# Performance work log

Hardware: AMD Instinct MI355X
Metric: run time of the kernel (lower is better)

The kernel has to match this reference:

```python
import jax, jax.numpy as jnp
import numpy as np

N_NODES = 50000
N_EDGES = 1600000
IN_FEAT = 128
HIDDEN = 128
NUM_CLASSES = 10
NUM_GRAPHS = 128


def setup_inputs() -> dict:
    key = jax.random.key(0)
    ks = jax.random.split(key, 10)
    x = jax.random.normal(ks[0], (N_NODES, IN_FEAT), dtype=jnp.float32)
    edge_index = jax.random.randint(ks[1], (2, N_EDGES), 0, N_NODES, dtype=jnp.int64)
    batch = jnp.sort(jax.random.randint(ks[2], (N_NODES,), 0, NUM_GRAPHS, dtype=jnp.int64))
    edge_mask = jax.random.uniform(ks[3], (N_EDGES,), dtype=jnp.float32)
    # Glorot-ish init for weights, zeros for biases (PyG default: glorot W, zero bias)
    def glorot(k, fan_in, fan_out):
        s = jnp.sqrt(6.0 / (fan_in + fan_out))
        return jax.random.uniform(k, (fan_in, fan_out), minval=-s, maxval=s, dtype=jnp.float32)
    W1 = glorot(ks[4], IN_FEAT, HIDDEN)
    b1 = jnp.zeros((HIDDEN,), dtype=jnp.float32)
    W2 = glorot(ks[5], HIDDEN, HIDDEN)
    b2 = jnp.zeros((HIDDEN,), dtype=jnp.float32)
    Wfc = glorot(ks[6], HIDDEN, NUM_CLASSES)
    bfc = jnp.zeros((NUM_CLASSES,), dtype=jnp.float32)
    return {"x": x, "edge_index": edge_index, "batch": batch, "edge_mask": edge_mask,
            "W1": W1, "b1": b1, "W2": W2, "b2": b2, "Wfc": Wfc, "bfc": bfc}


def _gcn_conv(x, W, b, edge_index, edge_weight, n_nodes):
    """PyG GCNConv: add self-loops (weight 1), symmetric deg^{-1/2} normalization,
    linear transform, gather-scatter aggregation source->target."""
    row, col = edge_index[0], edge_index[1]
    loop = jnp.arange(n_nodes, dtype=row.dtype)
    row = jnp.concatenate([row, loop])
    col = jnp.concatenate([col, loop])
    ew = jnp.concatenate([edge_weight, jnp.ones((n_nodes,), dtype=edge_weight.dtype)])
    deg = jax.ops.segment_sum(ew, col, num_segments=n_nodes)  # in-degree w.r.t. targets
    dinv = jnp.where(deg > 0, jax.lax.rsqrt(deg), 0.0)
    norm = dinv[row] * ew * dinv[col]                          # [E+N]
    h = x @ W                                                  # [N, out]
    msg = h[row] * norm[:, None]                               # gather + scale
    out = jax.ops.segment_sum(msg, col, num_segments=n_nodes)  # scatter-add
    return out + b


def reference(x, edge_index, batch, edge_mask, W1, b1, W2, b2, Wfc, bfc):
    n = x.shape[0]
    h = jax.nn.relu(_gcn_conv(x, W1, b1, edge_index, edge_mask, n))
    # dropout is identity in eval mode
    h = jax.nn.relu(_gcn_conv(h, W2, b2, edge_index, edge_mask, n))
    pooled = jax.ops.segment_sum(h, batch, num_segments=NUM_GRAPHS)  # global_add_pool
    logits = pooled @ Wfc + bfc
    return jax.nn.log_softmax(logits, axis=1)
```

## Files before the change

### kernel.cpp

```cpp
#include <hip/hip_runtime.h>
#include <hip/hip_bf16.h>

#define NN 50000
#define NE 1600000
#define FEAT 128
#define NG 128
#define NC 10

constexpr int SCAN_BLOCKS = (NN + 255) / 256;

typedef unsigned int u32x4 __attribute__((ext_vector_type(4)));
typedef short bf16x8 __attribute__((ext_vector_type(8)));
typedef float f32x4 __attribute__((ext_vector_type(4)));

__device__ __forceinline__ float bflo(unsigned u) { return __uint_as_float(u << 16); }
__device__ __forceinline__ float bfhi(unsigned u) { return __uint_as_float(u & 0xffff0000u); }
__device__ __forceinline__ float bfs(unsigned short u) { return __uint_as_float(((unsigned)u) << 16); }
__device__ __forceinline__ unsigned packbf(float a, float b) {
    unsigned ua = __float_as_uint(a), ub = __float_as_uint(b);
    ua += 0x7fffu + ((ua >> 16) & 1u);
    ub += 0x7fffu + ((ub >> 16) & 1u);
    return (ua >> 16) | (ub & 0xffff0000u);
}
__device__ __forceinline__ unsigned short bf1(float a) {
    unsigned ua = __float_as_uint(a);
    ua += 0x7fffu + ((ua >> 16) & 1u);
    return (unsigned short)(ua >> 16);
}

__global__ void k_rank(const int* __restrict__ col, int* __restrict__ counts,
                       int* __restrict__ rank) {
    int e = blockIdx.x * blockDim.x + threadIdx.x;
    if (e < NE) rank[e] = atomicAdd(&counts[col[e]], 1);
}

__global__ void k_scanA(const int* __restrict__ counts, int* __restrict__ offsets,
                        int* __restrict__ blockSums) {
    __shared__ int tmp[256];
    int i = blockIdx.x * 256 + threadIdx.x;
    int v = (i < NN) ? counts[i] : 0;
    tmp[threadIdx.x] = v;
    __syncthreads();
    for (int off = 1; off < 256; off <<= 1) {
        int t = (threadIdx.x >= off) ? tmp[threadIdx.x - off] : 0;
        __syncthreads();
        tmp[threadIdx.x] += t;
        __syncthreads();
    }
    if (i < NN) offsets[i] = tmp[threadIdx.x] - v;
    if (threadIdx.x == 255) blockSums[blockIdx.x] = tmp[255];
}

__global__ void k_scanB(int* __restrict__ blockSums) {
    __shared__ int tmp[256];
    int t = threadIdx.x;
    int v = (t < SCAN_BLOCKS) ? blockSums[t] : 0;
    tmp[t] = v;
    __syncthreads();
    for (int off = 1; off < 256; off <<= 1) {
        int u = (t >= off) ? tmp[t - off] : 0;
        __syncthreads();
        tmp[t] += u;
        __syncthreads();
    }
    if (t < SCAN_BLOCKS) blockSums[t] = tmp[t] - v;
}

__global__ void k_scanC(int* __restrict__ offsets, const int* __restrict__ blockSums) {
    int i = blockIdx.x * 256 + threadIdx.x;
    if (i < NN) offsets[i] += blockSums[blockIdx.x];
}

__global__ void k_fill(const int* __restrict__ row, const int* __restrict__ col,
                       const float* __restrict__ ew, const int* __restrict__ rank,
                       const int* __restrict__ offsets, long long* __restrict__ csr) {
    int e = blockIdx.x * blockDim.x + threadIdx.x;
    if (e < NE) {
        int pos = offsets[col[e]] + rank[e];
        long long v = (long long)(unsigned)row[e] | ((long long)__float_as_int(ew[e]) << 32);
        __builtin_nontemporal_store(v, csr + pos);
    }
}

__global__ void k_dinv2(const int* __restrict__ offsets, const int* __restrict__ counts,
                        const long long* __restrict__ csr, float* __restrict__ dinv) {
    int n = blockIdx.x * blockDim.x + threadIdx.x;
    if (n >= NN) return;
    int s = offsets[n], c = counts[n];
    float d = 0.f;
    for (int j = 0; j < c; ++j)
        d += __int_as_float((int)(csr[s + j] >> 32));
    dinv[n] = rsqrtf(d + 1.0f);
}

__global__ void k_cast(const float* __restrict__ x, unsigned short* __restrict__ xb) {
    size_t i = (size_t)(blockIdx.x * blockDim.x + threadIdx.x) * 8;
    const float4* p = (const float4*)(x + i);
    float4 v0 = p[0], v1 = p[1];
    u32x4 o;
    o.x = packbf(v0.x, v0.y); o.y = packbf(v0.z, v0.w);
    o.z = packbf(v1.x, v1.y); o.w = packbf(v1.z, v1.w);
    *(u32x4*)(xb + i) = o;
}

__global__ void k_prepW(const float* __restrict__ W, unsigned short* __restrict__ Wt) {
    int idx = blockIdx.x * 256 + threadIdx.x;
    int k = idx >> 7, n = idx & 127;
    Wt[n * 128 + k] = bf1(W[idx]);
}

__global__ __launch_bounds__(256) void k_gemm_mfma(const unsigned short* __restrict__ A,
                                                   const unsigned short* __restrict__ Wt,
                                                   const float* __restrict__ dinv,
                                                   unsigned short* __restrict__ C) {
    const int t = threadIdx.x;
    const int wid = t >> 6;
    const int lane = t & 63;
    const int row0 = blockIdx.x * 64 + wid * 16;
    const int l15 = lane & 15;
    const int kg = lane >> 4;

    int arow = row0 + l15;
    if (arow >= NN) arow = NN - 1;
    const unsigned short* ap = A + (size_t)arow * 128 + kg * 8;
    bf16x8 a[4];
#pragma unroll
    for (int ks = 0; ks < 4; ++ks)
        a[ks] = *(const bf16x8*)(ap + ks * 32);

    f32x4 acc[8];
#pragma unroll
    for (int ct = 0; ct < 8; ++ct) acc[ct] = (f32x4){0.f, 0.f, 0.f, 0.f};

#pragma unroll
    for (int ct = 0; ct < 8; ++ct) {
        const unsigned short* bp = Wt + (size_t)(ct * 16 + l15) * 128 + kg * 8;
#pragma unroll
        for (int ks = 0; ks < 4; ++ks) {
            bf16x8 b = *(const bf16x8*)(bp + ks * 32);
            acc[ct] = __builtin_amdgcn_mfma_f32_16x16x32_bf16(a[ks], b, acc[ct], 0, 0, 0);
        }
    }

    const int drow0 = row0 + kg * 4;
    float di[4];
#pragma unroll
    for (int r = 0; r < 4; ++r)
        di[r] = (drow0 + r < NN) ? dinv[drow0 + r] : 0.f;
#pragma unroll
    for (int ct = 0; ct < 8; ++ct) {
#pragma unroll
        for (int r = 0; r < 4; ++r) {
            int grow = drow0 + r;
            if (grow < NN)
                C[(size_t)grow * 128 + ct * 16 + l15] = bf1(acc[ct][r] * di[r]);
        }
    }
}

__global__ __launch_bounds__(256) void k_agg(const unsigned short* __restrict__ hs,
                                             const int* __restrict__ offsets,
                                             const int* __restrict__ counts,
                                             const long long* __restrict__ csr,
                                             const float* __restrict__ dinv,
                                             const float* __restrict__ bias,
                                             unsigned short* __restrict__ outb) {
    const int node = blockIdx.x * 4 + (threadIdx.x >> 6);
    if (node >= NN) return;
    const int lane = threadIdx.x & 63;
    const int qg = lane >> 4;
    const int fl = lane & 15;

    const int start = offsets[node];
    const int cnt = counts[node];
    const long long* ep = csr + start;
    const uint4* hb = (const uint4*)hs;

    float a0 = 0.f, a1 = 0.f, a2 = 0.f, a3 = 0.f;
    float a4 = 0.f, a5 = 0.f, a6 = 0.f, a7 = 0.f;

    auto fma8 = [&](uint4 v, float w) {
        a0 += bflo(v.x) * w; a1 += bfhi(v.x) * w;
        a2 += bflo(v.y) * w; a3 += bfhi(v.y) * w;
        a4 += bflo(v.z) * w; a5 += bfhi(v.z) * w;
        a6 += bflo(v.w) * w; a7 += bfhi(v.w) * w;
    };

    const int n16 = cnt >> 4;
    for (int i = 0; i < n16; ++i) {
        const int base = i * 16 + qg;
        long long l0 = __builtin_nontemporal_load(ep + base);
        long long l1 = __builtin_nontemporal_load(ep + base + 4);
        long long l2 = __builtin_nontemporal_load(ep + base + 8);
        long long l3 = __builtin_nontemporal_load(ep + base + 12);
        uint4 v0 = hb[(size_t)(int)l0 * 16 + fl];
        uint4 v1 = hb[(size_t)(int)l1 * 16 + fl];
        uint4 v2 = hb[(size_t)(int)l2 * 16 + fl];
        uint4 v3 = hb[(size_t)(int)l3 * 16 + fl];
        fma8(v0, __int_as_float((int)(l0 >> 32)));
        fma8(v1, __int_as_float((int)(l1 >> 32)));
        fma8(v2, __int_as_float((int)(l2 >> 32)));
        fma8(v3, __int_as_float((int)(l3 >> 32)));
    }
    for (int jj = n16 * 16; jj < cnt; jj += 4) {
        int idx = jj + qg;
        bool valid = idx < cnt;
        long long l = __builtin_nontemporal_load(ep + (valid ? idx : cnt - 1));
        float w = valid ? __int_as_float((int)(l >> 32)) : 0.f;
        uint4 v = hb[(size_t)(int)l * 16 + fl];
        fma8(v, w);
    }

    a0 += __shfl_xor(a0, 16); a0 += __shfl_xor(a0, 32);
    a1 += __shfl_xor(a1, 16); a1 += __shfl_xor(a1, 32);
    a2 += __shfl_xor(a2, 16); a2 += __shfl_xor(a2, 32);
    a3 += __shfl_xor(a3, 16); a3 += __shfl_xor(a3, 32);
    a4 += __shfl_xor(a4, 16); a4 += __shfl_xor(a4, 32);
    a5 += __shfl_xor(a5, 16); a5 += __shfl_xor(a5, 32);
    a6 += __shfl_xor(a6, 16); a6 += __shfl_xor(a6, 32);
    a7 += __shfl_xor(a7, 16); a7 += __shfl_xor(a7, 32);

    if (qg == 0) {
        uint4 sv = hb[(size_t)node * 16 + fl];
        fma8(sv, 1.0f);
        float di = dinv[node];
        float4 b0 = *(const float4*)(bias + fl * 8);
        float4 b1 = *(const float4*)(bias + fl * 8 + 4);
        a0 = fmaxf(di * a0 + b0.x, 0.f);
        a1 = fmaxf(di * a1 + b0.y, 0.f);
        a2 = fmaxf(di * a2 + b0.z, 0.f);
        a3 = fmaxf(di * a3 + b0.w, 0.f);
        a4 = fmaxf(di * a4 + b1.x, 0.f);
        a5 = fmaxf(di * a5 + b1.y, 0.f);
        a6 = fmaxf(di * a6 + b1.z, 0.f);
        a7 = fmaxf(di * a7 + b1.w, 0.f);
        u32x4 o;
        o.x = packbf(a0, a1); o.y = packbf(a2, a3);
        o.z = packbf(a4, a5); o.w = packbf(a6, a7);
        __builtin_nontemporal_store(o, (u32x4*)(outb + (size_t)node * 128 + fl * 8));
    }
}

__global__ __launch_bounds__(256) void k_pool(const unsigned short* __restrict__ h3,
                                              const int* __restrict__ batch,
                                              float* __restrict__ pooled) {
    __shared__ float sm[256];
    const int g = blockIdx.x;
    const int f = threadIdx.x & 127;
    const int half = threadIdx.x >> 7;
    int lo = 0, hi = NN;
    while (lo < hi) { int m = (lo + hi) >> 1; if (batch[m] < g) lo = m + 1; else hi = m; }
    int s0 = lo;
    hi = NN;
    while (lo < hi) { int m = (lo + hi) >> 1; if (batch[m] < g + 1) lo = m + 1; else hi = m; }
    int e0 = lo;

    float s = 0.f;
    int n = s0 + half;
    for (; n + 8 <= e0; n += 8) {
        s += bfs(h3[(size_t)n * 128 + f]);
        s += bfs(h3[(size_t)(n + 2) * 128 + f]);
        s += bfs(h3[(size_t)(n + 4) * 128 + f]);
        s += bfs(h3[(size_t)(n + 6) * 128 + f]);
    }
    for (; n < e0; n += 2) s += bfs(h3[(size_t)n * 128 + f]);

    sm[threadIdx.x] = s;
    __syncthreads();
    if (half == 0) pooled[(size_t)g * 128 + f] = sm[threadIdx.x] + sm[threadIdx.x + 128];
}

__global__ __launch_bounds__(64) void k_fc(const float* __restrict__ pooled,
                                           const float* __restrict__ Wfc,
                                           const float* __restrict__ bfc,
                                           float* __restrict__ out) {
    const int g = blockIdx.x;
    const int lane = threadIdx.x;
    float p0 = pooled[(size_t)g * 128 + lane];
    float p1 = pooled[(size_t)g * 128 + 64 + lane];
    float logits[NC];
#pragma unroll
    for (int c = 0; c < NC; ++c) {
        float v = p0 * Wfc[lane * NC + c] + p1 * Wfc[(64 + lane) * NC + c];
#pragma unroll
        for (int off = 32; off > 0; off >>= 1) v += __shfl_down(v, off);
        logits[c] = v;
    }
    if (lane == 0) {
        float mx = -1e30f;
#pragma unroll
        for (int c = 0; c < NC; ++c) { logits[c] += bfc[c]; mx = fmaxf(mx, logits[c]); }
        float s = 0.f;
#pragma unroll
        for (int c = 0; c < NC; ++c) s += expf(logits[c] - mx);
        float lse = mx + logf(s);
#pragma unroll
        for (int c = 0; c < NC; ++c) out[(size_t)g * NC + c] = logits[c] - lse;
    }
}

extern "C" void kernel_launch(void* const* d_in, const int* in_sizes, int n_in,
                              void* d_out, int out_size, void* d_ws, size_t ws_size,
                              hipStream_t stream) {
    const float* x         = (const float*)d_in[0];
    const int*   edge_index= (const int*)d_in[1];
    const int*   batch     = (const int*)d_in[2];
    const float* edge_mask = (const float*)d_in[3];
    const float* W1        = (const float*)d_in[4];
    const float* b1        = (const float*)d_in[5];
    const float* W2        = (const float*)d_in[6];
    const float* b2        = (const float*)d_in[7];
    const float* Wfc       = (const float*)d_in[8];
    const float* bfc       = (const float*)d_in[9];
    float* out = (float*)d_out;

    const int* row = edge_index;
    const int* col = edge_index + NE;

    char* ws = (char*)d_ws;
    size_t off = 0;
    auto alloc = [&](size_t bytes) -> void* {
        off = (off + 255) & ~(size_t)255;
        void* p = ws + off;
        off += bytes;
        return p;
    };
    int*   counts   = (int*)  alloc((size_t)NN * 4);
    int*   offsets  = (int*)  alloc((size_t)NN * 4);
    int*   blockSums= (int*)  alloc(256 * 4);
    float* dinv     = (float*)alloc((size_t)NN * 4);
    int*   rank     = (int*)  alloc((size_t)NE * 4);
    long long* csr  = (long long*)alloc((size_t)NE * 8);
    unsigned short* xb  = (unsigned short*)alloc((size_t)NN * FEAT * 2);
    unsigned short* hs1 = (unsigned short*)alloc((size_t)NN * FEAT * 2);
    unsigned short* h2  = (unsigned short*)alloc((size_t)NN * FEAT * 2);
    unsigned short* h3  = (unsigned short*)alloc((size_t)NN * FEAT * 2);
    unsigned short* Wt1 = (unsigned short*)alloc((size_t)FEAT * FEAT * 2);
    unsigned short* Wt2 = (unsigned short*)alloc((size_t)FEAT * FEAT * 2);
    float* pooled   = (float*)alloc((size_t)NG * FEAT * 4);

    hipMemsetAsync(counts, 0, (size_t)NN * 4, stream);

    k_rank<<<(NE + 255) / 256, 256, 0, stream>>>(col, counts, rank);
    k_scanA<<<SCAN_BLOCKS, 256, 0, stream>>>(counts, offsets, blockSums);
    k_scanB<<<1, 256, 0, stream>>>(blockSums);
    k_scanC<<<SCAN_BLOCKS, 256, 0, stream>>>(offsets, blockSums);
    k_fill<<<(NE + 255) / 256, 256, 0, stream>>>(row, col, edge_mask, rank, offsets, csr);
    k_dinv2<<<(NN + 255) / 256, 256, 0, stream>>>(offsets, counts, csr, dinv);

    k_cast<<<(NN * FEAT / 8 + 255) / 256, 256, 0, stream>>>(x, xb);
    k_prepW<<<64, 256, 0, stream>>>(W1, Wt1);
    k_prepW<<<64, 256, 0, stream>>>(W2, Wt2);

    k_gemm_mfma<<<(NN + 63) / 64, 256, 0, stream>>>(xb, Wt1, dinv, hs1);
    k_agg<<<(NN + 3) / 4, 256, 0, stream>>>(hs1, offsets, counts, csr, dinv, b1, h2);
    k_gemm_mfma<<<(NN + 63) / 64, 256, 0, stream>>>(h2, Wt2, dinv, hs1);
    k_agg<<<(NN + 3) / 4, 256, 0, stream>>>(hs1, offsets, counts, csr, dinv, b2, h3);
    k_pool<<<NG, 256, 0, stream>>>(h3, batch, pooled);
    k_fc<<<NG, 64, 0, stream>>>(pooled, Wfc, bfc, out);
}
```

Measured before the change: 439.2 us.

## Pad degree counters, fuse fp32 cast into GEMM, use offset-diff counts

Each per-node atomic degree counter now sits 64 bytes apart, so atomics from different nodes no longer share a cache line. The separate fp32-to-bf16 cast kernel is removed, and the first GEMM reads fp32 x directly and packs it to bf16 in registers. The CSR offsets array gets a sentinel entry so node degrees come from offset differences instead of the counts array, and the CSR fill uses regular rather than nontemporal stores. The trade-off is a 16x larger counters buffer to memset and scan with a strided read, and wider fp32 loads in the first GEMM.

```diff
diff --git a/kernel.cpp b/kernel.cpp
--- a/kernel.cpp
+++ b/kernel.cpp
@@ -6,6 +6,7 @@
 #define FEAT 128
 #define NG 128
 #define NC 10
+#define CPAD 16
 
 constexpr int SCAN_BLOCKS = (NN + 255) / 256;
 
@@ -31,14 +32,14 @@
 __global__ void k_rank(const int* __restrict__ col, int* __restrict__ counts,
                        int* __restrict__ rank) {
     int e = blockIdx.x * blockDim.x + threadIdx.x;
-    if (e < NE) rank[e] = atomicAdd(&counts[col[e]], 1);
+    if (e < NE) rank[e] = atomicAdd(&counts[(size_t)col[e] * CPAD], 1);
 }
 
 __global__ void k_scanA(const int* __restrict__ counts, int* __restrict__ offsets,
                         int* __restrict__ blockSums) {
     __shared__ int tmp[256];
     int i = blockIdx.x * 256 + threadIdx.x;
-    int v = (i < NN) ? counts[i] : 0;
+    int v = (i < NN) ? counts[(size_t)i * CPAD] : 0;
     tmp[threadIdx.x] = v;
     __syncthreads();
     for (int off = 1; off < 256; off <<= 1) {
@@ -69,6 +70,7 @@
 __global__ void k_scanC(int* __restrict__ offsets, const int* __restrict__ blockSums) {
     int i = blockIdx.x * 256 + threadIdx.x;
     if (i < NN) offsets[i] += blockSums[blockIdx.x];
+    if (i == 0) offsets[NN] = NE;
 }
 
 __global__ void k_fill(const int* __restrict__ row, const int* __restrict__ col,
@@ -78,29 +80,19 @@
     if (e < NE) {
         int pos = offsets[col[e]] + rank[e];
         long long v = (long long)(unsigned)row[e] | ((long long)__float_as_int(ew[e]) << 32);
-        __builtin_nontemporal_store(v, csr + pos);
-    }
-}
-
-__global__ void k_dinv2(const int* __restrict__ offsets, const int* __restrict__ counts,
-                        const long long* __restrict__ csr, float* __restrict__ dinv) {
+        csr[pos] = v;
+    }
+}
+
+__global__ void k_dinv2(const int* __restrict__ offsets, const long long* __restrict__ csr,
+                        float* __restrict__ dinv) {
     int n = blockIdx.x * blockDim.x + threadIdx.x;
     if (n >= NN) return;
-    int s = offsets[n], c = counts[n];
+    int s = offsets[n], e = offsets[n + 1];
     float d = 0.f;
-    for (int j = 0; j < c; ++j)
-        d += __int_as_float((int)(csr[s + j] >> 32));
+    for (int j = s; j < e; ++j)
+        d += __int_as_float((int)(csr[j] >> 32));
     dinv[n] = rsqrtf(d + 1.0f);
-}
-
-__global__ void k_cast(const float* __restrict__ x, unsigned short* __restrict__ xb) {
-    size_t i = (size_t)(blockIdx.x * blockDim.x + threadIdx.x) * 8;
-    const float4* p = (const float4*)(x + i);
-    float4 v0 = p[0], v1 = p[1];
-    u32x4 o;
-    o.x = packbf(v0.x, v0.y); o.y = packbf(v0.z, v0.w);
-    o.z = packbf(v1.x, v1.y); o.w = packbf(v1.z, v1.w);
-    *(u32x4*)(xb + i) = o;
 }
 
 __global__ void k_prepW(const float* __restrict__ W, unsigned short* __restrict__ Wt) {
@@ -109,7 +101,8 @@
     Wt[n * 128 + k] = bf1(W[idx]);
 }
 
-__global__ __launch_bounds__(256) void k_gemm_mfma(const unsigned short* __restrict__ A,
+template <typename TIN>
+__global__ __launch_bounds__(256) void k_gemm_mfma(const TIN* __restrict__ A,
                                                    const unsigned short* __restrict__ Wt,
                                                    const float* __restrict__ dinv,
                                                    unsigned short* __restrict__ C) {
@@ -122,11 +115,24 @@
 
     int arow = row0 + l15;
     if (arow >= NN) arow = NN - 1;
-    const unsigned short* ap = A + (size_t)arow * 128 + kg * 8;
     bf16x8 a[4];
-#pragma unroll
-    for (int ks = 0; ks < 4; ++ks)
-        a[ks] = *(const bf16x8*)(ap + ks * 32);
+    if constexpr (sizeof(TIN) == 2) {
+        const unsigned short* ap = (const unsigned short*)A + (size_t)arow * 128 + kg * 8;
+#pragma unroll
+        for (int ks = 0; ks < 4; ++ks)
+            a[ks] = *(const bf16x8*)(ap + ks * 32);
+    } else {
+        const float* ap = (const float*)A + (size_t)arow * 128 + kg * 8;
+#pragma unroll
+        for (int ks = 0; ks < 4; ++ks) {
+            float4 v0 = *(const float4*)(ap + ks * 32);
+            float4 v1 = *(const float4*)(ap + ks * 32 + 4);
+            u32x4 o;
+            o.x = packbf(v0.x, v0.y); o.y = packbf(v0.z, v0.w);
+            o.z = packbf(v1.x, v1.y); o.w = packbf(v1.z, v1.w);
+            a[ks] = __builtin_bit_cast(bf16x8, o);
+        }
+    }
 
     f32x4 acc[8];
 #pragma unroll
@@ -160,7 +166,6 @@
 
 __global__ __launch_bounds__(256) void k_agg(const unsigned short* __restrict__ hs,
                                              const int* __restrict__ offsets,
-                                             const int* __restrict__ counts,
                                              const long long* __restrict__ csr,
                                              const float* __restrict__ dinv,
                                              const float* __restrict__ bias,
@@ -172,7 +177,7 @@
     const int fl = lane & 15;
 
     const int start = offsets[node];
-    const int cnt = counts[node];
+    const int cnt = offsets[node + 1] - start;
     const long long* ep = csr + start;
     const uint4* hb = (const uint4*)hs;
 
@@ -325,13 +330,12 @@
         off += bytes;
         return p;
     };
-    int*   counts   = (int*)  alloc((size_t)NN * 4);
-    int*   offsets  = (int*)  alloc((size_t)NN * 4);
+    int*   counts   = (int*)  alloc((size_t)NN * CPAD * 4);
+    int*   offsets  = (int*)  alloc((size_t)(NN + 1) * 4);
     int*   blockSums= (int*)  alloc(256 * 4);
     float* dinv     = (float*)alloc((size_t)NN * 4);
     int*   rank     = (int*)  alloc((size_t)NE * 4);
     long long* csr  = (long long*)alloc((size_t)NE * 8);
-    unsigned short* xb  = (unsigned short*)alloc((size_t)NN * FEAT * 2);
     unsigned short* hs1 = (unsigned short*)alloc((size_t)NN * FEAT * 2);
     unsigned short* h2  = (unsigned short*)alloc((size_t)NN * FEAT * 2);
     unsigned short* h3  = (unsigned short*)alloc((size_t)NN * FEAT * 2);
@@ -339,23 +343,22 @@
     unsigned short* Wt2 = (unsigned short*)alloc((size_t)FEAT * FEAT * 2);
     float* pooled   = (float*)alloc((size_t)NG * FEAT * 4);
 
-    hipMemsetAsync(counts, 0, (size_t)NN * 4, stream);
+    hipMemsetAsync(counts, 0, (size_t)NN * CPAD * 4, stream);
 
     k_rank<<<(NE + 255) / 256, 256, 0, stream>>>(col, counts, rank);
     k_scanA<<<SCAN_BLOCKS, 256, 0, stream>>>(counts, offsets, blockSums);
     k_scanB<<<1, 256, 0, stream>>>(blockSums);
     k_scanC<<<SCAN_BLOCKS, 256, 0, stream>>>(offsets, blockSums);
     k_fill<<<(NE + 255) / 256, 256, 0, stream>>>(row, col, edge_mask, rank, offsets, csr);
-    k_dinv2<<<(NN + 255) / 256, 256, 0, stream>>>(offsets, counts, csr, dinv);
-
-    k_cast<<<(NN * FEAT / 8 + 255) / 256, 256, 0, stream>>>(x, xb);
+    k_dinv2<<<(NN + 255) / 256, 256, 0, stream>>>(offsets, csr, dinv);
+
     k_prepW<<<64, 256, 0, stream>>>(W1, Wt1);
     k_prepW<<<64, 256, 0, stream>>>(W2, Wt2);
 
-    k_gemm_mfma<<<(NN + 63) / 64, 256, 0, stream>>>(xb, Wt1, dinv, hs1);
-    k_agg<<<(NN + 3) / 4, 256, 0, stream>>>(hs1, offsets, counts, csr, dinv, b1, h2);
-    k_gemm_mfma<<<(NN + 63) / 64, 256, 0, stream>>>(h2, Wt2, dinv, hs1);
-    k_agg<<<(NN + 3) / 4, 256, 0, stream>>>(hs1, offsets, counts, csr, dinv, b2, h3);
+    k_gemm_mfma<float><<<(NN + 63) / 64, 256, 0, stream>>>(x, Wt1, dinv, hs1);
+    k_agg<<<(NN + 3) / 4, 256, 0, stream>>>(hs1, offsets, csr, dinv, b1, h2);
+    k_gemm_mfma<unsigned short><<<(NN + 63) / 64, 256, 0, stream>>>(h2, Wt2, dinv, hs1);
+    k_agg<<<(NN + 3) / 4, 256, 0, stream>>>(hs1, offsets, csr, dinv, b2, h3);
     k_pool<<<NG, 256, 0, stream>>>(h3, batch, pooled);
     k_fc<<<NG, 64, 0, stream>>>(pooled, Wfc, bfc, out);
 }
```

Measured after the change: 396.3 us. 9.8% less time.
